# Kernel tuning notes

Hardware: AMD Instinct MI355X
Metric: run time of the kernel (lower is better)

## Reference

```python
import jax, jax.numpy as jnp
import numpy as np

EPS = 1e-6
H = 8          # num_heads
GAMMA = 0.99   # fixed decay (requires_grad=False in source)
RPE_LAYERS = 3


def srms(x):
    # SimpleRMSNorm: x / (rms(x) + eps), rms = ||x||_2 / sqrt(d) = sqrt(mean(x^2))
    return x / (jnp.sqrt(jnp.mean(x * x, axis=-1, keepdims=True)) + EPS)


def setup_inputs() -> dict:
    key = jax.random.key(0)
    B, N, E = 8, 2048, 512
    D1 = 1536            # int(3*512) // 8 * 8
    R = 512              # rpe_embedding
    ks = jax.random.split(key, 12)

    def lin(k, i, o):
        return jax.random.normal(k, (i, o), jnp.float32) * (i ** -0.5)

    x = jax.random.normal(ks[0], (B, N, E), jnp.float32)
    return {
        "x": x,
        "Wu": lin(ks[1], E, D1), "bu": jnp.zeros((D1,), jnp.float32),
        "Wv": lin(ks[2], E, D1), "bv": jnp.zeros((D1,), jnp.float32),
        "Wo": lin(ks[3], D1, E), "bo": jnp.zeros((E,), jnp.float32),
        "rpe_Win": lin(ks[4], 1, R), "rpe_bin": jnp.zeros((R,), jnp.float32),
        "rpe_W": jax.random.normal(ks[5], (RPE_LAYERS, R, R), jnp.float32) * (R ** -0.5),
        "rpe_b": jnp.zeros((RPE_LAYERS, R), jnp.float32),
        "rpe_Wout": lin(ks[6], R, D1), "rpe_bout": jnp.zeros((D1,), jnp.float32),
    }


def reference(x, Wu, bu, Wv, bv, Wo, bo, rpe_Win, rpe_bin, rpe_W, rpe_b, rpe_Wout, rpe_bout):
    B, N, E = x.shape
    u = jax.nn.silu(x @ Wu + bu)                     # b n d1
    v = jax.nn.silu(x @ Wv + bv)                     # b n d1
    D1 = v.shape[-1]
    D = D1 // H
    v = v.reshape(B, N, H, D).transpose(0, 2, 1, 3)  # b h n d

    # RPE MLP over positions: row 0 is the zero index, rows 1..N-1 are pos indices 1..N-1 (par_type=1)
    idx = jnp.arange(0, N, dtype=x.dtype)[:, None]   # (N, 1)
    h = idx @ rpe_Win + rpe_bin                      # (N, R)
    for i in range(RPE_LAYERS):                      # residual=False
        h = jax.nn.relu(srms(h)) @ rpe_W[i] + rpe_b[i]
    coeffs = jax.nn.relu(srms(h)) @ rpe_Wout + rpe_bout   # (N, H*D)
    coeffs = coeffs.reshape(N, H, D).transpose(1, 0, 2)   # h n d

    zero = coeffs[:, :1]                             # h 1 d  (a_0)
    pos = coeffs[:, 1:]                              # h n-1 d (a_1..a_{n-1})
    decay = GAMMA ** jnp.arange(1, N, dtype=x.dtype)[None, :, None]
    pos = pos * decay
    # causal: a = [a0, a1..a_{n-1}, a0]; act_type='none' -> identity
    a = jnp.concatenate([zero, pos, zero], axis=1)   # h, n+1, d

    # Toeplitz mixing via circular convolution of length 2n (torch.fft.rfft/irfft, norm='backward')
    m = 2 * N
    yf = jnp.fft.rfft(v, m, axis=2)                  # b h m/2+1 d (complex)
    af = jnp.fft.rfft(a, m, axis=1)[None]            # 1 h m/2+1 d
    out = jnp.fft.irfft(yf * af, m, axis=2)[:, :, :N, :]  # b h n d

    out = out.transpose(0, 2, 1, 3).reshape(B, N, D1)     # b n (h d)
    out = u * out
    return out @ Wo + bo
```

## Files before the change

kernel.cpp:

```cpp
#include <hip/hip_runtime.h>
#include <cstdint>


typedef unsigned short ushort_t;
typedef __attribute__((ext_vector_type(8))) short short8;
typedef __attribute__((ext_vector_type(4))) float f32x4;

#define AS1 __attribute__((address_space(1)))
#define AS3 __attribute__((address_space(3)))

#define SW1(j) ((j) ^ (((j) >> 4) & 15))
#define SW2(j) ((j) ^ ((((j) >> 6) & 7) << 1))

__device__ __forceinline__ int xcd_swz(int bid, int nwg) {
  return (bid & 7) * (nwg >> 3) + (bid >> 3);
}

__device__ __forceinline__ float bf2f(ushort_t b) {
  union { unsigned u; float f; } x; x.u = ((unsigned)b) << 16; return x.f;
}
__device__ __forceinline__ ushort_t f2bf(float f) {
  union { float f; unsigned u; } x; x.f = f;
  unsigned r = x.u + 0x7fffu + ((x.u >> 16) & 1u);
  return (ushort_t)(r >> 16);
}

__device__ __forceinline__ void gload_lds16(const void* g, void* l) {
  auto gp = reinterpret_cast<const AS1 unsigned*>(reinterpret_cast<uintptr_t>(g));
  auto lp = reinterpret_cast<AS3 unsigned*>(reinterpret_cast<uintptr_t>(l));
  __builtin_amdgcn_global_load_lds(gp, lp, 16, 0, 0);
}

template<int MODE>
__launch_bounds__(256, 2)
__global__ void gemm_bt(const ushort_t* __restrict__ A, const ushort_t* __restrict__ Bt,
                        const float* __restrict__ bias, void* __restrict__ Cout,
                        void* __restrict__ Cout2, int M, int N, int K, float lng)
{
  __shared__ ushort_t As[128 * 64];
  __shared__ ushort_t Bs[128 * 64];
  const int tid  = threadIdx.x;
  const int wave = tid >> 6, lane = tid & 63;
  const int nb = N >> 7;
  const int lbid = xcd_swz((int)blockIdx.x, (int)gridDim.x);
  const int bm = lbid / nb, bn = lbid % nb;
  const int m0 = bm << 7, n0 = bn << 7;
  const int lrow = lane & 15, quad = lane >> 4;
  const int wm = (wave >> 1) << 6, wn = (wave & 1) << 6;
  const int srow = lane >> 3;
  const int scol = (lane & 7) << 3;

  f32x4 acc[4][4] = {};

  for (int kt = 0; kt < K; kt += 64) {
    __syncthreads();
#pragma unroll
    for (int i = 0; i < 4; ++i) {
      const int ci  = i * 4 + wave;
      const int row = ci * 8 + srow;
      gload_lds16(A  + (long)(m0 + row) * K + kt + scol, (void*)&As[ci * 512]);
      gload_lds16(Bt + (long)(n0 + row) * K + kt + scol, (void*)&Bs[ci * 512]);
    }
    __syncthreads();
#pragma unroll
    for (int s = 0; s < 2; ++s) {
      short8 afr[4], bfr[4];
#pragma unroll
      for (int i = 0; i < 4; ++i)
        afr[i] = *(const short8*)&As[(wm + i * 16 + lrow) * 64 + s * 32 + quad * 8];
#pragma unroll
      for (int j = 0; j < 4; ++j)
        bfr[j] = *(const short8*)&Bs[(wn + j * 16 + lrow) * 64 + s * 32 + quad * 8];
#pragma unroll
      for (int i = 0; i < 4; ++i)
#pragma unroll
        for (int j = 0; j < 4; ++j)
          acc[i][j] = __builtin_amdgcn_mfma_f32_16x16x32_bf16(afr[i], bfr[j], acc[i][j], 0, 0, 0);
    }
  }

#pragma unroll
  for (int i = 0; i < 4; ++i) {
    const int rowb = m0 + wm + i * 16 + quad * 4;
#pragma unroll
    for (int j = 0; j < 4; ++j) {
      const int col = n0 + wn + j * 16 + lrow;
      const float bv = bias[col];
      if (MODE == 0) {
#pragma unroll
        for (int r = 0; r < 4; ++r)
          ((float*)Cout)[(long)(rowb + r) * N + col] = acc[i][j][r] + bv;
      } else {
        if (col < 1536) {
#pragma unroll
          for (int r = 0; r < 4; ++r) {
            float val = acc[i][j][r] + bv;
            float sv = val / (1.f + __expf(-val));
            ((ushort_t*)Cout)[(long)(rowb + r) * 1536 + col] = f2bf(sv);
          }
        } else {
          union { ushort_t h[4]; uint2 u2; } pk;
#pragma unroll
          for (int r = 0; r < 4; ++r) {
            float val = acc[i][j][r] + bv;
            float sv = val / (1.f + __expf(-val));
            pk.h[r] = f2bf(sv);
          }
          *(uint2*)((ushort_t*)Cout2 + (long)(col - 1536) * 16384 + rowb) = pk.u2;
        }
      }
    }
  }
}

template<int MODE>
__launch_bounds__(256, 2)
__global__ void gemm64_bt(const ushort_t* __restrict__ A, const ushort_t* __restrict__ Bt,
                          const float* __restrict__ bias, float* __restrict__ Cout,
                          int M, int N, int K, float lng)
{
  __shared__ ushort_t As[64 * 64];
  __shared__ ushort_t Bs[64 * 64];
  const int tid = threadIdx.x, wave = tid >> 6, lane = tid & 63;
  const int nb = N >> 6;
  const int lbid = xcd_swz((int)blockIdx.x, (int)gridDim.x);
  const int bm = lbid / nb, bn = lbid % nb;
  const int m0 = bm << 6, n0 = bn << 6;
  const int lrow = lane & 15, quad = lane >> 4;
  const int wm = (wave >> 1) << 5, wn = (wave & 1) << 5;
  const int srow = lane >> 3, scol = (lane & 7) << 3;

  f32x4 acc[2][2] = {};

  for (int kt = 0; kt < K; kt += 64) {
    __syncthreads();
#pragma unroll
    for (int i = 0; i < 2; ++i) {
      const int ci = i * 4 + wave;
      const int row = ci * 8 + srow;
      gload_lds16(A  + (long)(m0 + row) * K + kt + scol, (void*)&As[ci * 512]);
      gload_lds16(Bt + (long)(n0 + row) * K + kt + scol, (void*)&Bs[ci * 512]);
    }
    __syncthreads();
#pragma unroll
    for (int s = 0; s < 2; ++s) {
      short8 afr[2], bfr[2];
#pragma unroll
      for (int i = 0; i < 2; ++i)
        afr[i] = *(const short8*)&As[(wm + i * 16 + lrow) * 64 + s * 32 + quad * 8];
#pragma unroll
      for (int j = 0; j < 2; ++j)
        bfr[j] = *(const short8*)&Bs[(wn + j * 16 + lrow) * 64 + s * 32 + quad * 8];
#pragma unroll
      for (int i = 0; i < 2; ++i)
#pragma unroll
        for (int j = 0; j < 2; ++j)
          acc[i][j] = __builtin_amdgcn_mfma_f32_16x16x32_bf16(afr[i], bfr[j], acc[i][j], 0, 0, 0);
    }
  }

#pragma unroll
  for (int i = 0; i < 2; ++i) {
    const int rowb = m0 + wm + i * 16 + quad * 4;
#pragma unroll
    for (int j = 0; j < 2; ++j) {
      const int col = n0 + wn + j * 16 + lrow;
      const float bv = bias[col];
#pragma unroll
      for (int r = 0; r < 4; ++r) {
        const int row = rowb + r;
        float val = acc[i][j][r] + bv;
        if (MODE == 0) Cout[(long)row * N + col] = val;
        else           Cout[(long)col * M + row] = val * __expf(lng * (float)row);
      }
    }
  }
}

__device__ __forceinline__ void srms_relu_store(float v0, float v1, ushort_t* out,
                                                long rowbase, int tid)
{
  float ss = v0 * v0 + v1 * v1;
#pragma unroll
  for (int off = 32; off; off >>= 1) ss += __shfl_down(ss, off);
  __shared__ float ps[4];
  const int wave = tid >> 6, lane = tid & 63;
  if (lane == 0) ps[wave] = ss;
  __syncthreads();
  float tot = ps[0] + ps[1] + ps[2] + ps[3];
  float sc = 1.f / (sqrtf(tot * (1.f / 512.f)) + 1e-6f);
  out[rowbase + tid]       = f2bf(fmaxf(v0 * sc, 0.f));
  out[rowbase + tid + 256] = f2bf(fmaxf(v1 * sc, 0.f));
}

__launch_bounds__(256)
__global__ void rpe_norm(const float* __restrict__ h, ushort_t* __restrict__ out)
{
  const int n = blockIdx.x, tid = threadIdx.x;
  float v0 = h[(long)n * 512 + tid];
  float v1 = h[(long)n * 512 + tid + 256];
  srms_relu_store(v0, v1, out, (long)n * 512, tid);
}

__device__ __forceinline__ void wtrans_body(const float* __restrict__ src,
                                            ushort_t* __restrict__ dst,
                                            int K, int N, int lb, int tid,
                                            float (*tile)[33])
{
  const int nbx = N >> 5;
  const int bx = lb % nbx, by = lb / nbx;
  const int n0 = bx << 5, k0 = by << 5;
  const int tx = tid & 31, ty = tid >> 5;
  for (int yy = ty; yy < 32; yy += 8)
    tile[yy][tx] = src[(long)(k0 + yy) * N + n0 + tx];
  __syncthreads();
  for (int yy = ty; yy < 32; yy += 8)
    dst[(long)(n0 + yy) * K + k0 + tx] = f2bf(tile[tx][yy]);
}

__launch_bounds__(256)
__global__ void prep_all(const float* __restrict__ Wu, const float* __restrict__ Wv,
                         const float* __restrict__ Wo, const float* __restrict__ rW,
                         const float* __restrict__ rWout,
                         const float* __restrict__ bu, const float* __restrict__ bv,
                         const float* __restrict__ x,
                         const float* __restrict__ rWin, const float* __restrict__ rbin,
                         ushort_t* __restrict__ wuvt, ushort_t* __restrict__ wot,
                         ushort_t* __restrict__ wrt, ushort_t* __restrict__ wroutt,
                         float* __restrict__ buvb, ushort_t* __restrict__ xb,
                         float2* __restrict__ twg, float2* __restrict__ twh,
                         ushort_t* __restrict__ a0)
{
  __shared__ float tile[32][33];
  const int bid = blockIdx.x, tid = threadIdx.x;
  if (bid < 3840) {
    const float* src; ushort_t* dst; int K, N, lb;
    if (bid < 768)       { src = Wu;    dst = wuvt;              K = 512;  N = 1536; lb = bid; }
    else if (bid < 1536) { src = Wv;    dst = wuvt + 1536L*512;  K = 512;  N = 1536; lb = bid - 768; }
    else if (bid < 2304) { src = Wo;    dst = wot;               K = 1536; N = 512;  lb = bid - 1536; }
    else if (bid < 2560) { src = rW;              dst = wrt;              K = 512; N = 512; lb = bid - 2304; }
    else if (bid < 2816) { src = rW + 512L*512;   dst = wrt + 512L*512;   K = 512; N = 512; lb = bid - 2560; }
    else if (bid < 3072) { src = rW + 2L*512*512; dst = wrt + 2L*512*512; K = 512; N = 512; lb = bid - 2816; }
    else                 { src = rWout; dst = wroutt;            K = 512;  N = 1536; lb = bid - 3072; }
    wtrans_body(src, dst, K, N, lb, tid, tile);
  } else if (bid < 3846) {
    int i = (bid - 3840) * 256 + tid;
    if (i < 1536) { buvb[i] = bu[i]; buvb[1536 + i] = bv[i]; }
  } else if (bid < 12038) {
    long i = (long)(bid - 3846) * 1024 + tid * 4;
    float4 f = *(const float4*)(x + i);
    unsigned lo = (unsigned)f2bf(f.x) | ((unsigned)f2bf(f.y) << 16);
    unsigned hi = (unsigned)f2bf(f.z) | ((unsigned)f2bf(f.w) << 16);
    *(uint2*)(xb + i) = make_uint2(lo, hi);
  } else if (bid < 12046) {
    int j = (bid - 12038) * 256 + tid;
    float s, c;
    __sincosf((float)j * (6.283185307179586f / 2048.f), &s, &c);
    twg[j] = make_float2(c, -s);
    float s2, c2;
    __sincosf((float)j * (3.14159265358979f / 2048.f), &s2, &c2);
    twh[j] = make_float2(c2, -s2);
  } else {
    const int n = bid - 12046;
    const float fn = (float)n;
    float v0 = fn * rWin[tid] + rbin[tid];
    float v1 = fn * rWin[tid + 256] + rbin[tid + 256];
    srms_relu_store(v0, v1, a0, (long)n * 512, tid);
  }
}

__device__ __forceinline__ float2 cmulf(float2 a, float2 b) {
  return make_float2(a.x * b.x - a.y * b.y, a.x * b.y + a.y * b.x);
}
__device__ __forceinline__ float4 c2add(float4 p, float4 q){
  return make_float4(p.x+q.x, p.y+q.y, p.z+q.z, p.w+q.w);
}
__device__ __forceinline__ float4 c2sub(float4 p, float4 q){
  return make_float4(p.x-q.x, p.y-q.y, p.z-q.z, p.w-q.w);
}
__device__ __forceinline__ float4 c2mni(float4 z){
  return make_float4(z.y, -z.x, z.w, -z.z);
}
__device__ __forceinline__ float4 c2w8(float4 z){
  const float s = 0.70710678118654752f;
  return make_float4(s*(z.x+z.y), s*(z.y-z.x), s*(z.z+z.w), s*(z.w-z.z));
}
__device__ __forceinline__ float4 c2w83(float4 z){
  const float s = 0.70710678118654752f;
  return make_float4(s*(z.y-z.x), -s*(z.x+z.y), s*(z.w-z.z), -s*(z.z+z.w));
}
__device__ __forceinline__ float4 c2mul(float4 z, float2 w){
  return make_float4(z.x*w.x - z.y*w.y, z.x*w.y + z.y*w.x,
                     z.z*w.x - z.w*w.y, z.z*w.y + z.w*w.x);
}

__device__ __forceinline__ void dft8d(const float4* u, float4* y)
{
  float4 a0=c2add(u[0],u[4]), a1=c2add(u[1],u[5]), a2=c2add(u[2],u[6]), a3=c2add(u[3],u[7]);
  float4 b0=c2sub(u[0],u[4]), b1=c2w8(c2sub(u[1],u[5])), b2=c2mni(c2sub(u[2],u[6])), b3=c2w83(c2sub(u[3],u[7]));
  float4 c0=c2add(a0,a2), c1=c2sub(a0,a2), c2=c2add(a1,a3), c3=c2mni(c2sub(a1,a3));
  y[0]=c2add(c0,c2); y[2]=c2add(c1,c3); y[4]=c2sub(c0,c2); y[6]=c2sub(c1,c3);
  float4 d0=c2add(b0,b2), d1=c2sub(b0,b2), d2=c2add(b1,b3), d3=c2mni(c2sub(b1,b3));
  y[1]=c2add(d0,d2); y[3]=c2add(d1,d3); y[5]=c2sub(d0,d2); y[7]=c2sub(d1,d3);
}
__device__ __forceinline__ void dft8d_hz(const float4* u, float4* y)
{
  float4 b1=c2w8(u[1]), b2=c2mni(u[2]), b3=c2w83(u[3]);
  float4 c0=c2add(u[0],u[2]), c1=c2sub(u[0],u[2]), c2=c2add(u[1],u[3]), c3=c2mni(c2sub(u[1],u[3]));
  y[0]=c2add(c0,c2); y[2]=c2add(c1,c3); y[4]=c2sub(c0,c2); y[6]=c2sub(c1,c3);
  float4 d0=c2add(u[0],b2), d1=c2sub(u[0],b2), d2=c2add(b1,b3), d3=c2mni(c2sub(b1,b3));
  y[1]=c2add(d0,d2); y[3]=c2add(d1,d3); y[5]=c2sub(d0,d2); y[7]=c2sub(d1,d3);
}

template<bool HZ>
__device__ void fft2048_ip4(float4* b, const float2* __restrict__ tw, int tid)
{
  float4 u[8], y[8];
  {
    const int i = tid;
#pragma unroll
    for (int m = 0; m < (HZ ? 4 : 8); ++m) u[m] = b[i + 256*m];
    if (HZ) dft8d_hz(u, y); else dft8d(u, y);
    __syncthreads();
    const int j = i << 3;
#pragma unroll
    for (int m = 0; m < 8; ++m) b[SW1(j + m)] = y[m];
  }
  __syncthreads();
  {
    const int i = tid, k = i & 7, tb = k << 5;
    float2 w[8];
#pragma unroll
    for (int m = 1; m < 8; ++m) w[m] = tw[m * tb];
#pragma unroll
    for (int m = 0; m < 8; ++m) u[m] = b[SW1(i + 256*m)];
#pragma unroll
    for (int m = 1; m < 8; ++m) u[m] = c2mul(u[m], w[m]);
    dft8d(u, y);
    __syncthreads();
    const int j = ((i - k) << 3) + k;
#pragma unroll
    for (int m = 0; m < 8; ++m) b[SW2(j + 8*m)] = y[m];
  }
  __syncthreads();
  {
    const int i = tid, k = i & 63, tb = k << 2;
    float2 w[8];
#pragma unroll
    for (int m = 1; m < 8; ++m) w[m] = tw[m * tb];
#pragma unroll
    for (int m = 0; m < 8; ++m) u[m] = b[SW2(i + 256*m)];
#pragma unroll
    for (int m = 1; m < 8; ++m) u[m] = c2mul(u[m], w[m]);
    dft8d(u, y);
    __syncthreads();
    const int j = ((i - k) << 3) + k;
#pragma unroll
    for (int m = 0; m < 8; ++m) b[j + 64*m] = y[m];
  }
  __syncthreads();
#pragma unroll
  for (int hh = 0; hh < 2; ++hh) {
    const int i = tid + (hh << 8);
    float2 w1 = tw[i], w2 = tw[2 * i], w3 = tw[3 * i];
    float4 q0 = b[i], q1 = b[i + 512], q2 = b[i + 1024], q3 = b[i + 1536];
    q1 = c2mul(q1, w1); q2 = c2mul(q2, w2); q3 = c2mul(q3, w3);
    float4 v0 = c2add(q0, q2), v2 = c2sub(q0, q2);
    float4 v1 = c2add(q1, q3), v3 = c2mni(c2sub(q1, q3));
    b[i]        = c2add(v0, v1);
    b[i + 512]  = c2add(v2, v3);
    b[i + 1024] = c2sub(v0, v1);
    b[i + 1536] = c2sub(v2, v3);
  }
  __syncthreads();
}

__launch_bounds__(256, 4)
__global__ void fft_kernel_spec(const float* __restrict__ kern, float2* __restrict__ af,
                                const float2* __restrict__ twg, const float2* __restrict__ twh)
{
  __shared__ float4 bx[2048];
  const int tid = threadIdx.x;
  const int c0 = (int)blockIdx.x * 2;
  const float* ka = kern + (long)c0 * 2048;
  const float* kb = ka + 2048;
  for (int j = tid; j < 1024; j += 256) {
    float2 A = *(const float2*)(ka + 2 * j);
    float2 B = *(const float2*)(kb + 2 * j);
    bx[j] = make_float4(A.x, A.y, B.x, B.y);
  }
  __syncthreads();
  fft2048_ip4<true>(bx, twg, tid);
  float2* af0 = af + (long)c0 * 2052;
  float2* af1 = af0 + 2052;
  for (int k = tid; k <= 1024; k += 256) {
    const float2 W = twh[k];
    const int kn = (2048 - k) & 2047;
    const float4 Zk4 = bx[k], Zn4 = bx[kn];
    {
      float2 Zk = make_float2(Zk4.x, Zk4.y), Zn = make_float2(Zn4.x, Zn4.y);
      float2 E = make_float2(0.5f * (Zk.x + Zn.x), 0.5f * (Zk.y - Zn.y));
      float2 O = make_float2(0.5f * (Zk.y + Zn.y), 0.5f * (Zn.x - Zk.x));
      float2 WO = cmulf(W, O);
      af0[k] = make_float2(E.x + WO.x, E.y + WO.y);
      if (k != 0 && k != 1024) af0[2048 - k] = make_float2(E.x - WO.x, -(E.y - WO.y));
      if (k == 0)              af0[2048]     = make_float2(E.x - WO.x, -(E.y - WO.y));
    }
    {
      float2 Zk = make_float2(Zk4.z, Zk4.w), Zn = make_float2(Zn4.z, Zn4.w);
      float2 E = make_float2(0.5f * (Zk.x + Zn.x), 0.5f * (Zk.y - Zn.y));
      float2 O = make_float2(0.5f * (Zk.y + Zn.y), 0.5f * (Zn.x - Zk.x));
      float2 WO = cmulf(W, O);
      af1[k] = make_float2(E.x + WO.x, E.y + WO.y);
      if (k != 0 && k != 1024) af1[2048 - k] = make_float2(E.x - WO.x, -(E.y - WO.y));
      if (k == 0)              af1[2048]     = make_float2(E.x - WO.x, -(E.y - WO.y));
    }
  }
}

__launch_bounds__(256, 4)
__global__ void fft_conv(ushort_t* __restrict__ vt, const float2* __restrict__ af,
                         const float2* __restrict__ twg, const float2* __restrict__ twh)
{
  __shared__ float4 bx[2048];
  const int tid = threadIdx.x;
  const long s0 = (long)blockIdx.x * 2;
  const int c = (int)(s0 >> 3);
  ushort_t* vsa = vt + s0 * 2048;
  ushort_t* vsb = vsa + 2048;
#pragma unroll
  for (int jj = 0; jj < 4; ++jj) {
    const int j = tid + jj * 256;
    unsigned pa = *(const unsigned*)(vsa + 2 * j);
    unsigned pb = *(const unsigned*)(vsb + 2 * j);
    bx[j] = make_float4(bf2f((ushort_t)(pa & 0xffffu)), bf2f((ushort_t)(pa >> 16)),
                        bf2f((ushort_t)(pb & 0xffffu)), bf2f((ushort_t)(pb >> 16)));
  }
  __syncthreads();
  fft2048_ip4<true>(bx, twg, tid);
  const float2* afc = af + (long)c * 2052;
  for (int k = tid; k <= 1024; k += 256) {
    const float2 A0 = afc[k], A1 = afc[2048 - k], W = twh[k];
    const float2 cW = make_float2(W.x, -W.y);
    const int kn = (2048 - k) & 2047;
    const float4 Zk4 = bx[k], Zn4 = bx[kn];
    float2 ya0, yn0, ya1, yn1;
    {
      float2 Zk = make_float2(Zk4.x, Zk4.y), Zn = make_float2(Zn4.x, Zn4.y);
      float2 E = make_float2(0.5f * (Zk.x + Zn.x), 0.5f * (Zk.y - Zn.y));
      float2 O = make_float2(0.5f * (Zk.y + Zn.y), 0.5f * (Zn.x - Zk.x));
      float2 WO = cmulf(W, O);
      float2 Xk = make_float2(E.x + WO.x, E.y + WO.y);
      float2 Xn = make_float2(E.x - WO.x, -(E.y - WO.y));
      float2 Pk = cmulf(Xk, A0);
      float2 Pn = cmulf(Xn, A1);
      float2 E2 = make_float2(0.5f * (Pk.x + Pn.x), 0.5f * (Pk.y - Pn.y));
      float2 G  = make_float2(0.5f * (Pk.x - Pn.x), 0.5f * (Pk.y + Pn.y));
      float2 Fo = cmulf(cW, G);
      ya0 = make_float2(E2.x - Fo.y, -(E2.y + Fo.x));
      yn0 = make_float2(E2.x + Fo.y, E2.y - Fo.x);
    }
    {
      float2 Zk = make_float2(Zk4.z, Zk4.w), Zn = make_float2(Zn4.z, Zn4.w);
      float2 E = make_float2(0.5f * (Zk.x + Zn.x), 0.5f * (Zk.y - Zn.y));
      float2 O = make_float2(0.5f * (Zk.y + Zn.y), 0.5f * (Zn.x - Zk.x));
      float2 WO = cmulf(W, O);
      float2 Xk = make_float2(E.x + WO.x, E.y + WO.y);
      float2 Xn = make_float2(E.x - WO.x, -(E.y - WO.y));
      float2 Pk = cmulf(Xk, A0);
      float2 Pn = cmulf(Xn, A1);
      float2 E2 = make_float2(0.5f * (Pk.x + Pn.x), 0.5f * (Pk.y - Pn.y));
      float2 G  = make_float2(0.5f * (Pk.x - Pn.x), 0.5f * (Pk.y + Pn.y));
      float2 Fo = cmulf(cW, G);
      ya1 = make_float2(E2.x - Fo.y, -(E2.y + Fo.x));
      yn1 = make_float2(E2.x + Fo.y, E2.y - Fo.x);
    }
    bx[k] = make_float4(ya0.x, ya0.y, ya1.x, ya1.y);
    if (k != 0 && k != 1024)
      bx[2048 - k] = make_float4(yn0.x, yn0.y, yn1.x, yn1.y);
  }
  __syncthreads();
  fft2048_ip4<false>(bx, twg, tid);
  const float inv = 1.f / 2048.f;
#pragma unroll
  for (int jj = 0; jj < 4; ++jj) {
    const int j = tid + jj * 256;
    float4 r = bx[j];
    unsigned oa = (unsigned)f2bf(r.x * inv) | ((unsigned)f2bf(-r.y * inv) << 16);
    unsigned ob = (unsigned)f2bf(r.z * inv) | ((unsigned)f2bf(-r.w * inv) << 16);
    *(unsigned*)(vsa + 2 * j) = oa;
    *(unsigned*)(vsb + 2 * j) = ob;
  }
}

__launch_bounds__(256)
__global__ void gate_trans(const ushort_t* __restrict__ convt, ushort_t* __restrict__ u)
{
  __shared__ ushort_t tile[64][65];
  const int bc = (int)blockIdx.x % 24, br = (int)blockIdx.x / 24;
  const int c0 = bc << 6, r0 = br << 6;
  const int tx = threadIdx.x & 63, ty = threadIdx.x >> 6;
  for (int yy = ty; yy < 64; yy += 4)
    tile[yy][tx] = convt[(long)(c0 + yy) * 16384 + r0 + tx];
  __syncthreads();
  for (int yy = ty; yy < 64; yy += 4) {
    long ui = (long)(r0 + yy) * 1536 + c0 + tx;
    float uu = bf2f(u[ui]);
    float cc = bf2f(tile[tx][yy]);
    u[ui] = f2bf(uu * cc);
  }
}

extern "C" void kernel_launch(void* const* d_in, const int* in_sizes, int n_in,
                              void* d_out, int out_size, void* d_ws, size_t ws_size,
                              hipStream_t stream)
{
  const float* x     = (const float*)d_in[0];
  const float* Wu    = (const float*)d_in[1];
  const float* bu    = (const float*)d_in[2];
  const float* Wv    = (const float*)d_in[3];
  const float* bv    = (const float*)d_in[4];
  const float* Wo    = (const float*)d_in[5];
  const float* bo    = (const float*)d_in[6];
  const float* rWin  = (const float*)d_in[7];
  const float* rbin  = (const float*)d_in[8];
  const float* rW    = (const float*)d_in[9];
  const float* rb    = (const float*)d_in[10];
  const float* rWout = (const float*)d_in[11];
  const float* rbout = (const float*)d_in[12];

  char* base = (char*)d_ws;
  size_t off = 0;
  auto alloc = [&](size_t bytes) -> char* {
    size_t r = (off + 255) & ~(size_t)255; off = r + bytes; return base + r;
  };
  ushort_t* wuvt   = (ushort_t*)alloc(3072L * 512 * 2);
  ushort_t* wot    = (ushort_t*)alloc(512L * 1536 * 2);
  ushort_t* wrt    = (ushort_t*)alloc(3L * 512 * 512 * 2);
  ushort_t* wroutt = (ushort_t*)alloc(1536L * 512 * 2);
  float*    buvb   = (float*)   alloc(3072L * 4);
  ushort_t* a0     = (ushort_t*)alloc(2048L * 512 * 2);
  float2*   af     = (float2*)  alloc(1536L * 2052 * 8);
  float2*   twg    = (float2*)  alloc(2048L * 8);
  float2*   twh    = (float2*)  alloc(2048L * 8);
  char*     X      = alloc(16384L * 512 * 2);
  ushort_t* u      = (ushort_t*)alloc(16384L * 1536 * 2);
  ushort_t* vt     = (ushort_t*)alloc(1536L * 16384 * 2);
  ushort_t* xb   = (ushort_t*)X;
  float*    h    = (float*)X;
  float*    kern = (float*)(X + 4L * 1024 * 1024);

  const float lng = -0.01005033585350145f;

  prep_all<<<dim3(14094), dim3(256), 0, stream>>>(
      Wu, Wv, Wo, rW, rWout, bu, bv, x, rWin, rbin,
      wuvt, wot, wrt, wroutt, buvb, xb, twg, twh, a0);

  gemm_bt<3><<<dim3(3072), dim3(256), 0, stream>>>(xb, wuvt, buvb, u, vt,
                                                   16384, 3072, 512, 0.f);

  for (int i = 0; i < 3; ++i) {
    gemm64_bt<0><<<dim3(256), dim3(256), 0, stream>>>(a0, wrt + (long)i * 512 * 512,
                                                      rb + (long)i * 512, h,
                                                      2048, 512, 512, 0.f);
    rpe_norm<<<dim3(2048), dim3(256), 0, stream>>>(h, a0);
  }
  gemm64_bt<2><<<dim3(768), dim3(256), 0, stream>>>(a0, wroutt, rbout, kern,
                                                    2048, 1536, 512, lng);
  fft_kernel_spec<<<dim3(768), dim3(256), 0, stream>>>(kern, af, twg, twh);

  fft_conv<<<dim3(6144), dim3(256), 0, stream>>>(vt, af, twg, twh);
  gate_trans<<<dim3(6144), dim3(256), 0, stream>>>(vt, u);
  gemm_bt<0><<<dim3(512), dim3(256), 0, stream>>>(u, wot, bo, d_out, nullptr,
                                                  16384, 512, 1536, 0.f);
}
```

Measured before the change: 448.7 us.

## Restructure 2048-point FFT as radix-4 split plus per-wave 512-point FFTs

Replaces the block-wide 2048-point FFT (four stages with block barriers) with an initial radix-4 decimation-in-frequency pass done while loading, followed by four independent 512-point FFTs, one per wavefront. Those sub-FFTs synchronize only with LDS wait fences instead of __syncthreads. The spectral pointwise step is rewritten to index the digit-reversed layout directly. The inverse FFT runs a matching radix-4 pass and writes output with 16-byte stores. This removes block-wide barriers and simplifies the swizzle, but the indexing is more intricate and relies on wave-local LDS ordering.

Measured after the change: 482.6 us. 1.08x slower.

```diff
diff --git a/kernel.cpp b/kernel.cpp
--- a/kernel.cpp
+++ b/kernel.cpp
@@ -9,8 +9,7 @@
 #define AS1 __attribute__((address_space(1)))
 #define AS3 __attribute__((address_space(3)))
 
-#define SW1(j) ((j) ^ (((j) >> 4) & 15))
-#define SW2(j) ((j) ^ ((((j) >> 6) & 7) << 1))
+#define SW5(j) ((j) ^ (((j) >> 3) & 7))
 
 __device__ __forceinline__ int xcd_swz(int bid, int nwg) {
   return (bid & 7) * (nwg >> 3) + (bid >> 3);
@@ -281,6 +280,9 @@
 __device__ __forceinline__ float4 c2mni(float4 z){
   return make_float4(z.y, -z.x, z.w, -z.z);
 }
+__device__ __forceinline__ float4 c2pi(float4 z){
+  return make_float4(-z.y, z.x, -z.w, z.z);
+}
 __device__ __forceinline__ float4 c2w8(float4 z){
   const float s = 0.70710678118654752f;
   return make_float4(s*(z.x+z.y), s*(z.y-z.x), s*(z.z+z.w), s*(z.w-z.z));
@@ -303,108 +305,104 @@
   float4 d0=c2add(b0,b2), d1=c2sub(b0,b2), d2=c2add(b1,b3), d3=c2mni(c2sub(b1,b3));
   y[1]=c2add(d0,d2); y[3]=c2add(d1,d3); y[5]=c2sub(d0,d2); y[7]=c2sub(d1,d3);
 }
-__device__ __forceinline__ void dft8d_hz(const float4* u, float4* y)
-{
-  float4 b1=c2w8(u[1]), b2=c2mni(u[2]), b3=c2w83(u[3]);
-  float4 c0=c2add(u[0],u[2]), c1=c2sub(u[0],u[2]), c2=c2add(u[1],u[3]), c3=c2mni(c2sub(u[1],u[3]));
-  y[0]=c2add(c0,c2); y[2]=c2add(c1,c3); y[4]=c2sub(c0,c2); y[6]=c2sub(c1,c3);
-  float4 d0=c2add(u[0],b2), d1=c2sub(u[0],b2), d2=c2add(b1,b3), d3=c2mni(c2sub(b1,b3));
-  y[1]=c2add(d0,d2); y[3]=c2add(d1,d3); y[5]=c2sub(d0,d2); y[7]=c2sub(d1,d3);
-}
-
-template<bool HZ>
-__device__ void fft2048_ip4(float4* b, const float2* __restrict__ tw, int tid)
+
+__device__ __forceinline__ void lds_fence() {
+  asm volatile("s_waitcnt lgkmcnt(0)" ::: "memory");
+  __builtin_amdgcn_sched_barrier(0);
+}
+
+__device__ void fft512_wave(float4* R, const float2* __restrict__ tw, int l)
 {
   float4 u[8], y[8];
   {
-    const int i = tid;
-#pragma unroll
-    for (int m = 0; m < (HZ ? 4 : 8); ++m) u[m] = b[i + 256*m];
-    if (HZ) dft8d_hz(u, y); else dft8d(u, y);
-    __syncthreads();
-    const int j = i << 3;
-#pragma unroll
-    for (int m = 0; m < 8; ++m) b[SW1(j + m)] = y[m];
-  }
-  __syncthreads();
-  {
-    const int i = tid, k = i & 7, tb = k << 5;
-    float2 w[8];
-#pragma unroll
-    for (int m = 1; m < 8; ++m) w[m] = tw[m * tb];
-#pragma unroll
-    for (int m = 0; m < 8; ++m) u[m] = b[SW1(i + 256*m)];
-#pragma unroll
-    for (int m = 1; m < 8; ++m) u[m] = c2mul(u[m], w[m]);
+#pragma unroll
+    for (int m = 0; m < 8; ++m) u[m] = R[l + 64*m];
     dft8d(u, y);
-    __syncthreads();
-    const int j = ((i - k) << 3) + k;
-#pragma unroll
-    for (int m = 0; m < 8; ++m) b[SW2(j + 8*m)] = y[m];
-  }
-  __syncthreads();
-  {
-    const int i = tid, k = i & 63, tb = k << 2;
-    float2 w[8];
-#pragma unroll
-    for (int m = 1; m < 8; ++m) w[m] = tw[m * tb];
-#pragma unroll
-    for (int m = 0; m < 8; ++m) u[m] = b[SW2(i + 256*m)];
-#pragma unroll
-    for (int m = 1; m < 8; ++m) u[m] = c2mul(u[m], w[m]);
+    lds_fence();
+    const int j = l << 3;
+#pragma unroll
+    for (int m = 0; m < 8; ++m) R[SW5(j + m)] = y[m];
+  }
+  lds_fence();
+  {
+    const int k = l & 7, tb = k << 5;
+    float2 ww[8];
+#pragma unroll
+    for (int m = 1; m < 8; ++m) ww[m] = tw[m * tb];
+#pragma unroll
+    for (int m = 0; m < 8; ++m) u[m] = R[SW5(l + 64*m)];
+#pragma unroll
+    for (int m = 1; m < 8; ++m) u[m] = c2mul(u[m], ww[m]);
     dft8d(u, y);
-    __syncthreads();
-    const int j = ((i - k) << 3) + k;
-#pragma unroll
-    for (int m = 0; m < 8; ++m) b[j + 64*m] = y[m];
-  }
-  __syncthreads();
-#pragma unroll
-  for (int hh = 0; hh < 2; ++hh) {
-    const int i = tid + (hh << 8);
-    float2 w1 = tw[i], w2 = tw[2 * i], w3 = tw[3 * i];
-    float4 q0 = b[i], q1 = b[i + 512], q2 = b[i + 1024], q3 = b[i + 1536];
-    q1 = c2mul(q1, w1); q2 = c2mul(q2, w2); q3 = c2mul(q3, w3);
-    float4 v0 = c2add(q0, q2), v2 = c2sub(q0, q2);
-    float4 v1 = c2add(q1, q3), v3 = c2mni(c2sub(q1, q3));
-    b[i]        = c2add(v0, v1);
-    b[i + 512]  = c2add(v2, v3);
-    b[i + 1024] = c2sub(v0, v1);
-    b[i + 1536] = c2sub(v2, v3);
-  }
-  __syncthreads();
+    lds_fence();
+    const int j = ((l - k) << 3) + k;
+#pragma unroll
+    for (int m = 0; m < 8; ++m) R[j + 8*m] = y[m];
+  }
+  lds_fence();
+  {
+    const int tb = l << 2;
+    float2 ww[8];
+#pragma unroll
+    for (int m = 1; m < 8; ++m) ww[m] = tw[m * tb];
+#pragma unroll
+    for (int m = 0; m < 8; ++m) u[m] = R[l + 64*m];
+#pragma unroll
+    for (int m = 1; m < 8; ++m) u[m] = c2mul(u[m], ww[m]);
+    dft8d(u, y);
+    lds_fence();
+#pragma unroll
+    for (int m = 0; m < 8; ++m) R[l + 64*m] = y[m];
+  }
+  lds_fence();
 }
 
 __launch_bounds__(256, 4)
 __global__ void fft_kernel_spec(const float* __restrict__ kern, float2* __restrict__ af,
                                 const float2* __restrict__ twg, const float2* __restrict__ twh)
 {
-  __shared__ float4 bx[2048];
+  __shared__ float4 b[2048];
   const int tid = threadIdx.x;
+  const int lane = tid & 63, w = tid >> 6;
   const int c0 = (int)blockIdx.x * 2;
   const float* ka = kern + (long)c0 * 2048;
   const float* kb = ka + 2048;
-  for (int j = tid; j < 1024; j += 256) {
-    float2 A = *(const float2*)(ka + 2 * j);
-    float2 B = *(const float2*)(kb + 2 * j);
-    bx[j] = make_float4(A.x, A.y, B.x, B.y);
-  }
-  __syncthreads();
-  fft2048_ip4<true>(bx, twg, tid);
+
+#pragma unroll
+  for (int h = 0; h < 2; ++h) {
+    const int n1 = tid + (h << 8);
+    float2 A0v = *(const float2*)(ka + 2*n1);
+    float2 A1v = *(const float2*)(ka + 2*(n1+512));
+    float2 B0v = *(const float2*)(kb + 2*n1);
+    float2 B1v = *(const float2*)(kb + 2*(n1+512));
+    float4 x0 = make_float4(A0v.x, A0v.y, B0v.x, B0v.y);
+    float4 x1 = make_float4(A1v.x, A1v.y, B1v.x, B1v.y);
+    float2 w1 = twg[n1], w2 = twg[2*n1], w3 = twg[3*n1];
+    b[n1]        = c2add(x0, x1);
+    b[512 + n1]  = c2mul(c2add(x0, c2mni(x1)), w1);
+    b[1024 + n1] = c2mul(c2sub(x0, x1), w2);
+    b[1536 + n1] = c2mul(c2add(x0, c2pi(x1)), w3);
+  }
+  __syncthreads();
+  fft512_wave(b + (w << 9), twg, lane);
+  __syncthreads();
+
   float2* af0 = af + (long)c0 * 2052;
   float2* af1 = af0 + 2052;
-  for (int k = tid; k <= 1024; k += 256) {
+#pragma unroll
+  for (int s = 0; s < 4; ++s) {
+    const int k = 4*tid + s;
+    const int kn = (2048 - k) & 2047;
+    const float4 Zk4 = b[s*512 + tid];
+    const float4 Zn4 = b[(kn & 3)*512 + (kn >> 2)];
     const float2 W = twh[k];
-    const int kn = (2048 - k) & 2047;
-    const float4 Zk4 = bx[k], Zn4 = bx[kn];
     {
       float2 Zk = make_float2(Zk4.x, Zk4.y), Zn = make_float2(Zn4.x, Zn4.y);
       float2 E = make_float2(0.5f * (Zk.x + Zn.x), 0.5f * (Zk.y - Zn.y));
       float2 O = make_float2(0.5f * (Zk.y + Zn.y), 0.5f * (Zn.x - Zk.x));
       float2 WO = cmulf(W, O);
       af0[k] = make_float2(E.x + WO.x, E.y + WO.y);
-      if (k != 0 && k != 1024) af0[2048 - k] = make_float2(E.x - WO.x, -(E.y - WO.y));
-      if (k == 0)              af0[2048]     = make_float2(E.x - WO.x, -(E.y - WO.y));
+      af0[2048 - k] = make_float2(E.x - WO.x, -(E.y - WO.y));
     }
     {
       float2 Zk = make_float2(Zk4.z, Zk4.w), Zn = make_float2(Zn4.z, Zn4.w);
@@ -412,8 +410,25 @@
       float2 O = make_float2(0.5f * (Zk.y + Zn.y), 0.5f * (Zn.x - Zk.x));
       float2 WO = cmulf(W, O);
       af1[k] = make_float2(E.x + WO.x, E.y + WO.y);
-      if (k != 0 && k != 1024) af1[2048 - k] = make_float2(E.x - WO.x, -(E.y - WO.y));
-      if (k == 0)              af1[2048]     = make_float2(E.x - WO.x, -(E.y - WO.y));
+      af1[2048 - k] = make_float2(E.x - WO.x, -(E.y - WO.y));
+    }
+  }
+  if (tid == 0) {
+    const float4 Z4 = b[256];
+    const float2 W = twh[1024];
+    {
+      float2 Zk = make_float2(Z4.x, Z4.y);
+      float2 E = make_float2(Zk.x, 0.f);
+      float2 O = make_float2(Zk.y, 0.f);
+      float2 WO = cmulf(W, O);
+      af0[1024] = make_float2(E.x + WO.x, E.y + WO.y);
+    }
+    {
+      float2 Zk = make_float2(Z4.z, Z4.w);
+      float2 E = make_float2(Zk.x, 0.f);
+      float2 O = make_float2(Zk.y, 0.f);
+      float2 WO = cmulf(W, O);
+      af1[1024] = make_float2(E.x + WO.x, E.y + WO.y);
     }
   }
 }
@@ -422,28 +437,46 @@
 __global__ void fft_conv(ushort_t* __restrict__ vt, const float2* __restrict__ af,
                          const float2* __restrict__ twg, const float2* __restrict__ twh)
 {
-  __shared__ float4 bx[2048];
+  __shared__ float4 b[2048];
   const int tid = threadIdx.x;
+  const int lane = tid & 63, w = tid >> 6;
   const long s0 = (long)blockIdx.x * 2;
   const int c = (int)(s0 >> 3);
   ushort_t* vsa = vt + s0 * 2048;
   ushort_t* vsb = vsa + 2048;
-#pragma unroll
-  for (int jj = 0; jj < 4; ++jj) {
-    const int j = tid + jj * 256;
-    unsigned pa = *(const unsigned*)(vsa + 2 * j);
-    unsigned pb = *(const unsigned*)(vsb + 2 * j);
-    bx[j] = make_float4(bf2f((ushort_t)(pa & 0xffffu)), bf2f((ushort_t)(pa >> 16)),
-                        bf2f((ushort_t)(pb & 0xffffu)), bf2f((ushort_t)(pb >> 16)));
-  }
-  __syncthreads();
-  fft2048_ip4<true>(bx, twg, tid);
+
+#pragma unroll
+  for (int h = 0; h < 2; ++h) {
+    const int n1 = tid + (h << 8);
+    unsigned pa0 = *(const unsigned*)(vsa + 2*n1);
+    unsigned pa1 = *(const unsigned*)(vsa + 2*(n1+512));
+    unsigned pb0 = *(const unsigned*)(vsb + 2*n1);
+    unsigned pb1 = *(const unsigned*)(vsb + 2*(n1+512));
+    float4 x0 = make_float4(bf2f((ushort_t)(pa0 & 0xffffu)), bf2f((ushort_t)(pa0 >> 16)),
+                            bf2f((ushort_t)(pb0 & 0xffffu)), bf2f((ushort_t)(pb0 >> 16)));
+    float4 x1 = make_float4(bf2f((ushort_t)(pa1 & 0xffffu)), bf2f((ushort_t)(pa1 >> 16)),
+                            bf2f((ushort_t)(pb1 & 0xffffu)), bf2f((ushort_t)(pb1 >> 16)));
+    float2 w1 = twg[n1], w2 = twg[2*n1], w3 = twg[3*n1];
+    b[n1]        = c2add(x0, x1);
+    b[512 + n1]  = c2mul(c2add(x0, c2mni(x1)), w1);
+    b[1024 + n1] = c2mul(c2sub(x0, x1), w2);
+    b[1536 + n1] = c2mul(c2add(x0, c2pi(x1)), w3);
+  }
+  __syncthreads();
+  fft512_wave(b + (w << 9), twg, lane);
+  __syncthreads();
+
   const float2* afc = af + (long)c * 2052;
-  for (int k = tid; k <= 1024; k += 256) {
+#pragma unroll
+  for (int s = 0; s < 4; ++s) {
+    const int k = 4*tid + s;
+    const int kn = (2048 - k) & 2047;
+    const int ofk = s*512 + tid;
+    const int ofn = (kn & 3)*512 + (kn >> 2);
+    const float4 Zk4 = b[ofk];
+    const float4 Zn4 = b[ofn];
     const float2 A0 = afc[k], A1 = afc[2048 - k], W = twh[k];
     const float2 cW = make_float2(W.x, -W.y);
-    const int kn = (2048 - k) & 2047;
-    const float4 Zk4 = bx[k], Zn4 = bx[kn];
     float2 ya0, yn0, ya1, yn1;
     {
       float2 Zk = make_float2(Zk4.x, Zk4.y), Zn = make_float2(Zn4.x, Zn4.y);
@@ -475,22 +508,100 @@
       ya1 = make_float2(E2.x - Fo.y, -(E2.y + Fo.x));
       yn1 = make_float2(E2.x + Fo.y, E2.y - Fo.x);
     }
-    bx[k] = make_float4(ya0.x, ya0.y, ya1.x, ya1.y);
-    if (k != 0 && k != 1024)
-      bx[2048 - k] = make_float4(yn0.x, yn0.y, yn1.x, yn1.y);
-  }
-  __syncthreads();
-  fft2048_ip4<false>(bx, twg, tid);
+    b[ofk] = make_float4(ya0.x, ya0.y, ya1.x, ya1.y);
+    if (k != 0)
+      b[ofn] = make_float4(yn0.x, yn0.y, yn1.x, yn1.y);
+  }
+  if (tid == 0) {
+    const float4 Z4 = b[256];
+    const float2 A0 = afc[1024], W = twh[1024];
+    const float2 cW = make_float2(W.x, -W.y);
+    float2 ya0, ya1;
+    {
+      float2 Zk = make_float2(Z4.x, Z4.y);
+      float2 E = make_float2(Zk.x, 0.f);
+      float2 O = make_float2(Zk.y, 0.f);
+      float2 WO = cmulf(W, O);
+      float2 Xk = make_float2(E.x + WO.x, E.y + WO.y);
+      float2 Xn = make_float2(E.x - WO.x, -(E.y - WO.y));
+      float2 Pk = cmulf(Xk, A0);
+      float2 Pn = cmulf(Xn, A0);
+      float2 E2 = make_float2(0.5f * (Pk.x + Pn.x), 0.5f * (Pk.y - Pn.y));
+      float2 G  = make_float2(0.5f * (Pk.x - Pn.x), 0.5f * (Pk.y + Pn.y));
+      float2 Fo = cmulf(cW, G);
+      ya0 = make_float2(E2.x - Fo.y, -(E2.y + Fo.x));
+    }
+    {
+      float2 Zk = make_float2(Z4.z, Z4.w);
+      float2 E = make_float2(Zk.x, 0.f);
+      float2 O = make_float2(Zk.y, 0.f);
+      float2 WO = cmulf(W, O);
+      float2 Xk = make_float2(E.x + WO.x, E.y + WO.y);
+      float2 Xn = make_float2(E.x - WO.x, -(E.y - WO.y));
+      float2 Pk = cmulf(Xk, A0);
+      float2 Pn = cmulf(Xn, A0);
+      float2 E2 = make_float2(0.5f * (Pk.x + Pn.x), 0.5f * (Pk.y - Pn.y));
+      float2 G  = make_float2(0.5f * (Pk.x - Pn.x), 0.5f * (Pk.y + Pn.y));
+      float2 Fo = cmulf(cW, G);
+      ya1 = make_float2(E2.x - Fo.y, -(E2.y + Fo.x));
+    }
+    b[256] = make_float4(ya0.x, ya0.y, ya1.x, ya1.y);
+  }
+  __syncthreads();
+
+  float4 q0a, q1a, q2a, q3a, q0b, q1b, q2b, q3b;
+  {
+    const int n1 = tid;
+    const int base = (n1 & 3)*512 + (n1 >> 2);
+    q0a = b[base]; q1a = b[base + 128]; q2a = b[base + 256]; q3a = b[base + 384];
+  }
+  {
+    const int n1 = tid + 256;
+    const int base = (n1 & 3)*512 + (n1 >> 2);
+    q0b = b[base]; q1b = b[base + 128]; q2b = b[base + 256]; q3b = b[base + 384];
+  }
+  __syncthreads();
+#pragma unroll
+  for (int h = 0; h < 2; ++h) {
+    const int n1 = tid + (h << 8);
+    float4 q0 = h ? q0b : q0a, q1 = h ? q1b : q1a;
+    float4 q2 = h ? q2b : q2a, q3 = h ? q3b : q3a;
+    float2 w1 = twg[n1], w2 = twg[2*n1], w3 = twg[3*n1];
+    float4 e0 = c2add(q0, q2), e1 = c2sub(q0, q2);
+    float4 o0 = c2add(q1, q3), o1 = c2sub(q1, q3);
+    b[n1]        = c2add(e0, o0);
+    b[512 + n1]  = c2mul(c2add(e1, c2mni(o1)), w1);
+    b[1024 + n1] = c2mul(c2sub(e0, o0), w2);
+    b[1536 + n1] = c2mul(c2add(e1, c2pi(o1)), w3);
+  }
+  __syncthreads();
+  fft512_wave(b + (w << 9), twg, lane);
+  __syncthreads();
+
   const float inv = 1.f / 2048.f;
-#pragma unroll
-  for (int jj = 0; jj < 4; ++jj) {
-    const int j = tid + jj * 256;
-    float4 r = bx[j];
-    unsigned oa = (unsigned)f2bf(r.x * inv) | ((unsigned)f2bf(-r.y * inv) << 16);
-    unsigned ob = (unsigned)f2bf(r.z * inv) | ((unsigned)f2bf(-r.w * inv) << 16);
-    *(unsigned*)(vsa + 2 * j) = oa;
-    *(unsigned*)(vsb + 2 * j) = ob;
-  }
+  uint4 oa, ob;
+  {
+    float4 r = b[tid];
+    oa.x = (unsigned)f2bf(r.x * inv) | ((unsigned)f2bf(-r.y * inv) << 16);
+    ob.x = (unsigned)f2bf(r.z * inv) | ((unsigned)f2bf(-r.w * inv) << 16);
+  }
+  {
+    float4 r = b[512 + tid];
+    oa.y = (unsigned)f2bf(r.x * inv) | ((unsigned)f2bf(-r.y * inv) << 16);
+    ob.y = (unsigned)f2bf(r.z * inv) | ((unsigned)f2bf(-r.w * inv) << 16);
+  }
+  {
+    float4 r = b[1024 + tid];
+    oa.z = (unsigned)f2bf(r.x * inv) | ((unsigned)f2bf(-r.y * inv) << 16);
+    ob.z = (unsigned)f2bf(r.z * inv) | ((unsigned)f2bf(-r.w * inv) << 16);
+  }
+  {
+    float4 r = b[1536 + tid];
+    oa.w = (unsigned)f2bf(r.x * inv) | ((unsigned)f2bf(-r.y * inv) << 16);
+    ob.w = (unsigned)f2bf(r.z * inv) | ((unsigned)f2bf(-r.w * inv) << 16);
+  }
+  *(uint4*)(vsa + 8*tid) = oa;
+  *(uint4*)(vsb + 8*tid) = ob;
 }
 
 __launch_bounds__(256)
```

## Fuse RPE MLP layers and output projection into one kernel

Applied to the files above, without the earlier changes.

Replaces the three per-layer GEMM plus SimpleRMSNorm launches and the output-projection GEMM with a single kernel. Each block keeps 16 position rows resident in LDS across all layers and computes the row norm in-register via shuffles and a small shared reduction. This removes seven launches and the fp32 round trips of the hidden activations through global memory. In exchange only 128 blocks run, and the weights are read directly from global memory without LDS tiling, so each block re-reads all weight matrices.

Result: slower. 507.2 us (+13.0%).

```diff
diff --git a/kernel.cpp b/kernel.cpp
--- a/kernel.cpp
+++ b/kernel.cpp
@@ -113,66 +113,102 @@
   }
 }
 
-template<int MODE>
-__launch_bounds__(256, 2)
-__global__ void gemm64_bt(const ushort_t* __restrict__ A, const ushort_t* __restrict__ Bt,
-                          const float* __restrict__ bias, float* __restrict__ Cout,
-                          int M, int N, int K, float lng)
-{
-  __shared__ ushort_t As[64 * 64];
-  __shared__ ushort_t Bs[64 * 64];
+__launch_bounds__(512, 1)
+__global__ void rpe_chain(const ushort_t* __restrict__ a0g,
+                          const ushort_t* __restrict__ wrt,
+                          const float* __restrict__ rb,
+                          const ushort_t* __restrict__ wroutt,
+                          const float* __restrict__ rbout,
+                          float* __restrict__ kern, float lng)
+{
+  __shared__ ushort_t As[16 * 520];
+  __shared__ float ps[8][16];
   const int tid = threadIdx.x, wave = tid >> 6, lane = tid & 63;
-  const int nb = N >> 6;
-  const int lbid = xcd_swz((int)blockIdx.x, (int)gridDim.x);
-  const int bm = lbid / nb, bn = lbid % nb;
-  const int m0 = bm << 6, n0 = bn << 6;
   const int lrow = lane & 15, quad = lane >> 4;
-  const int wm = (wave >> 1) << 5, wn = (wave & 1) << 5;
-  const int srow = lane >> 3, scol = (lane & 7) << 3;
-
-  f32x4 acc[2][2] = {};
-
-  for (int kt = 0; kt < K; kt += 64) {
-    __syncthreads();
-#pragma unroll
-    for (int i = 0; i < 2; ++i) {
-      const int ci = i * 4 + wave;
-      const int row = ci * 8 + srow;
-      gload_lds16(A  + (long)(m0 + row) * K + kt + scol, (void*)&As[ci * 512]);
-      gload_lds16(Bt + (long)(n0 + row) * K + kt + scol, (void*)&Bs[ci * 512]);
-    }
-    __syncthreads();
-#pragma unroll
-    for (int s = 0; s < 2; ++s) {
-      short8 afr[2], bfr[2];
-#pragma unroll
-      for (int i = 0; i < 2; ++i)
-        afr[i] = *(const short8*)&As[(wm + i * 16 + lrow) * 64 + s * 32 + quad * 8];
-#pragma unroll
-      for (int j = 0; j < 2; ++j)
-        bfr[j] = *(const short8*)&Bs[(wn + j * 16 + lrow) * 64 + s * 32 + quad * 8];
-#pragma unroll
-      for (int i = 0; i < 2; ++i)
-#pragma unroll
-        for (int j = 0; j < 2; ++j)
-          acc[i][j] = __builtin_amdgcn_mfma_f32_16x16x32_bf16(afr[i], bfr[j], acc[i][j], 0, 0, 0);
-    }
-  }
-
-#pragma unroll
-  for (int i = 0; i < 2; ++i) {
-    const int rowb = m0 + wm + i * 16 + quad * 4;
-#pragma unroll
-    for (int j = 0; j < 2; ++j) {
-      const int col = n0 + wn + j * 16 + lrow;
+  const int n0 = (int)blockIdx.x << 4;
+
+#pragma unroll
+  for (int it = 0; it < 2; ++it) {
+    const int idx = it * 512 + tid;
+    const int row = idx >> 6, cg = idx & 63;
+    *(uint4*)&As[row * 520 + cg * 8] =
+        *(const uint4*)&a0g[(long)(n0 + row) * 512 + cg * 8];
+  }
+  __syncthreads();
+
+  for (int L = 0; L < 3; ++L) {
+    const ushort_t* W = wrt + (long)L * 512 * 512;
+    const float* bias = rb + L * 512;
+    f32x4 acc[4] = {};
+#pragma unroll 4
+    for (int kt = 0; kt < 512; kt += 32) {
+      short8 af = *(const short8*)&As[lrow * 520 + kt + quad * 8];
+#pragma unroll
+      for (int j = 0; j < 4; ++j) {
+        const int col = (wave << 6) + j * 16 + lrow;
+        short8 bf = *(const short8*)&W[(long)col * 512 + kt + quad * 8];
+        acc[j] = __builtin_amdgcn_mfma_f32_16x16x32_bf16(af, bf, acc[j], 0, 0, 0);
+      }
+    }
+    float ssr[4] = {0.f, 0.f, 0.f, 0.f};
+#pragma unroll
+    for (int j = 0; j < 4; ++j) {
+      const int col = (wave << 6) + j * 16 + lrow;
       const float bv = bias[col];
 #pragma unroll
       for (int r = 0; r < 4; ++r) {
-        const int row = rowb + r;
-        float val = acc[i][j][r] + bv;
-        if (MODE == 0) Cout[(long)row * N + col] = val;
-        else           Cout[(long)col * M + row] = val * __expf(lng * (float)row);
+        float val = acc[j][r] + bv;
+        acc[j][r] = val;
+        ssr[r] += val * val;
       }
+    }
+#pragma unroll
+    for (int m = 1; m < 16; m <<= 1)
+#pragma unroll
+      for (int r = 0; r < 4; ++r) ssr[r] += __shfl_xor(ssr[r], m);
+    if (lrow == 0) {
+#pragma unroll
+      for (int r = 0; r < 4; ++r) ps[wave][quad * 4 + r] = ssr[r];
+    }
+    __syncthreads();
+#pragma unroll
+    for (int r = 0; r < 4; ++r) {
+      const int row = quad * 4 + r;
+      float tot = ps[0][row] + ps[1][row] + ps[2][row] + ps[3][row]
+                + ps[4][row] + ps[5][row] + ps[6][row] + ps[7][row];
+      float sc = 1.f / (sqrtf(tot * (1.f / 512.f)) + 1e-6f);
+#pragma unroll
+      for (int j = 0; j < 4; ++j) {
+        const int col = (wave << 6) + j * 16 + lrow;
+        As[row * 520 + col] = f2bf(fmaxf(acc[j][r] * sc, 0.f));
+      }
+    }
+    __syncthreads();
+  }
+
+  for (int p = 0; p < 3; ++p) {
+    f32x4 acc[4] = {};
+#pragma unroll 4
+    for (int kt = 0; kt < 512; kt += 32) {
+      short8 af = *(const short8*)&As[lrow * 520 + kt + quad * 8];
+#pragma unroll
+      for (int j = 0; j < 4; ++j) {
+        const int col = (p << 9) + (wave << 6) + j * 16 + lrow;
+        short8 bf = *(const short8*)&wroutt[(long)col * 512 + kt + quad * 8];
+        acc[j] = __builtin_amdgcn_mfma_f32_16x16x32_bf16(af, bf, acc[j], 0, 0, 0);
+      }
+    }
+#pragma unroll
+    for (int j = 0; j < 4; ++j) {
+      const int col = (p << 9) + (wave << 6) + j * 16 + lrow;
+      const float bv = rbout[col];
+      const int nb = n0 + quad * 4;
+      float4 o;
+      o.x = (acc[j][0] + bv) * __expf(lng * (float)(nb));
+      o.y = (acc[j][1] + bv) * __expf(lng * (float)(nb + 1));
+      o.z = (acc[j][2] + bv) * __expf(lng * (float)(nb + 2));
+      o.w = (acc[j][3] + bv) * __expf(lng * (float)(nb + 3));
+      *(float4*)&kern[(long)col * 2048 + nb] = o;
     }
   }
 }
@@ -191,15 +227,6 @@
   float sc = 1.f / (sqrtf(tot * (1.f / 512.f)) + 1e-6f);
   out[rowbase + tid]       = f2bf(fmaxf(v0 * sc, 0.f));
   out[rowbase + tid + 256] = f2bf(fmaxf(v1 * sc, 0.f));
-}
-
-__launch_bounds__(256)
-__global__ void rpe_norm(const float* __restrict__ h, ushort_t* __restrict__ out)
-{
-  const int n = blockIdx.x, tid = threadIdx.x;
-  float v0 = h[(long)n * 512 + tid];
-  float v1 = h[(long)n * 512 + tid + 256];
-  srms_relu_store(v0, v1, out, (long)n * 512, tid);
 }
 
 __device__ __forceinline__ void wtrans_body(const float* __restrict__ src,
@@ -547,7 +574,6 @@
   ushort_t* u      = (ushort_t*)alloc(16384L * 1536 * 2);
   ushort_t* vt     = (ushort_t*)alloc(1536L * 16384 * 2);
   ushort_t* xb   = (ushort_t*)X;
-  float*    h    = (float*)X;
   float*    kern = (float*)(X + 4L * 1024 * 1024);
 
   const float lng = -0.01005033585350145f;
@@ -559,14 +585,8 @@
   gemm_bt<3><<<dim3(3072), dim3(256), 0, stream>>>(xb, wuvt, buvb, u, vt,
                                                    16384, 3072, 512, 0.f);
 
-  for (int i = 0; i < 3; ++i) {
-    gemm64_bt<0><<<dim3(256), dim3(256), 0, stream>>>(a0, wrt + (long)i * 512 * 512,
-                                                      rb + (long)i * 512, h,
-                                                      2048, 512, 512, 0.f);
-    rpe_norm<<<dim3(2048), dim3(256), 0, stream>>>(h, a0);
-  }
-  gemm64_bt<2><<<dim3(768), dim3(256), 0, stream>>>(a0, wroutt, rbout, kern,
-                                                    2048, 1536, 512, lng);
+  rpe_chain<<<dim3(128), dim3(512), 0, stream>>>(a0, wrt, rb, wroutt, rbout,
+                                                 kern, lng);
   fft_kernel_spec<<<dim3(768), dim3(256), 0, stream>>>(kern, af, twg, twh);
 
   fft_conv<<<dim3(6144), dim3(256), 0, stream>>>(vt, af, twg, twh);
```
